# Performance work log

Hardware: AMD Instinct MI355X
Metric: run time of the kernel (lower is better)

Reference implementation:

```python
import jax, jax.numpy as jnp
import numpy as np

K = 8192
C = 512
BETA = 0.25
DECAY = 0.99
EPS = 1e-05


def setup_inputs() -> dict:
    key = jax.random.key(0)
    k1, k2, k3 = jax.random.split(key, 3)
    z_e = jax.random.normal(k1, (8, 1024, C), dtype=jnp.float32)
    codebook = jax.random.normal(k2, (K, C), dtype=jnp.float32) * 0.02
    cluster_size = jax.random.uniform(k3, (K,), dtype=jnp.float32)
    embed_avg = codebook  # buffer initialized as a copy of the codebook
    return {"z_e": z_e, "codebook": codebook, "cluster_size": cluster_size, "embed_avg": embed_avg}


def reference(z_e, codebook, cluster_size, embed_avg):
    B, N, Cc = z_e.shape
    z = z_e.reshape(-1, Cc)            # [T, C]
    z32 = z.astype(jnp.float32)
    cw = codebook.astype(jnp.float32)  # [K, C]

    # squared L2 distances: ||z||^2 - 2 z.e + ||e||^2  -> [T, K]
    dist = (jnp.sum(z32 * z32, axis=1, keepdims=True)
            - 2.0 * (z32 @ cw.T)
            + jnp.sum(cw * cw, axis=1)[None, :])
    idx = jnp.argmin(dist, axis=1)     # [T]
    z_q = cw[idx]                      # [T, C] gather

    vq_loss = BETA * jnp.mean((z32 - jax.lax.stop_gradient(z_q)) ** 2)

    # straight-through estimator
    z_st = z + jax.lax.stop_gradient(z_q.astype(z.dtype) - z)
    z_q_st = z_st.reshape(B, N, Cc)
    indices = idx.reshape(B, N)

    # EMA codebook update (training path; no_grad in original)
    counts = jax.ops.segment_sum(jnp.ones(idx.shape, jnp.float32), idx, num_segments=K)
    embed_sum = jax.ops.segment_sum(z32, idx, num_segments=K)  # [K, C] scatter-add
    new_cluster_size = cluster_size * DECAY + counts * (1.0 - DECAY)
    new_embed_avg = embed_avg * DECAY + embed_sum * (1.0 - DECAY)
    n = jnp.maximum(jnp.sum(new_cluster_size), 1.0)
    smoothed = (new_cluster_size + EPS) / (n + K * EPS) * n
    new_codebook = new_embed_avg / smoothed[:, None]

    return z_q_st, indices, vq_loss, new_codebook, new_cluster_size, new_embed_avg
```

## Files before the change

kernel.cpp:

```cpp
#include <hip/hip_runtime.h>
#include <cstdint>
#include <cstddef>

#define T_TOK 8192
#define K_CODE 8192
#define C_DIM 512
#define BETA 0.25f
#define DECAY 0.99f
#define ONE_MINUS_DECAY 0.01f
#define EPS_F 1e-5f
#define K_EPS 0.08192f
#define MARGIN 0.0625f

#define ZQ_OFF   ((size_t)0)
#define IDX_OFF  ((size_t)4194304)
#define LOSS_OFF ((size_t)4202496)
#define NCB_OFF  ((size_t)4202497)
#define NCS_OFF  ((size_t)8396801)
#define NEA_OFF  ((size_t)8404993)

#define CP_F_OFF    ((size_t)2097152)
#define SLAB1_F_OFF ((size_t)8404994)
#define SLAB2_F_OFF ((size_t)(8404994 + 524288))
#define LOSSP_F_OFF ((size_t)9453570)
#define LIST_I_OFF  ((size_t)10502146)
#define OFFSA_I_OFF ((size_t)10510338)
#define OFFSB_I_OFF ((size_t)10518530)

#define WS_ZNORM  0
#define WS_ENORM  8192
#define WS_ICOUNT 16384
#define WS_NSUM   24576

typedef _Float16 half8 __attribute__((ext_vector_type(8)));
typedef _Float16 half4v __attribute__((ext_vector_type(4)));
typedef float floatx4 __attribute__((ext_vector_type(4)));
typedef unsigned long long ull;

__device__ __forceinline__ void gload16(const void* g, void* l) {
    __builtin_amdgcn_global_load_lds(
        (const __attribute__((address_space(1))) void*)g,
        (__attribute__((address_space(3))) void*)l, 16, 0, 0);
}

__device__ __forceinline__ unsigned umin32(unsigned a, unsigned b) { return a < b ? a : b; }
__device__ __forceinline__ unsigned umax32(unsigned a, unsigned b) { return a > b ? a : b; }

__device__ __forceinline__ float dot8(float4 z0, float4 z1, float4 c0, float4 c1) {
    float p = 0.0f;
    p = fmaf(z0.x, c0.x, p); p = fmaf(z0.y, c0.y, p);
    p = fmaf(z0.z, c0.z, p); p = fmaf(z0.w, c0.w, p);
    p = fmaf(z1.x, c1.x, p); p = fmaf(z1.y, c1.y, p);
    p = fmaf(z1.z, c1.z, p); p = fmaf(z1.w, c1.w, p);
    return p;
}

__global__ __launch_bounds__(256) void prep_kernel(const float* __restrict__ z,
                                                   const float* __restrict__ cb,
                                                   _Float16* __restrict__ zp,
                                                   _Float16* __restrict__ cp,
                                                   float* __restrict__ ws) {
    int tid = threadIdx.x;
    int row = blockIdx.x * 2 + (tid >> 7);
    int l128 = tid & 127;
    const float* src;
    _Float16* dst;
    float* nrm;
    if (row < T_TOK) { src = z + (size_t)row * C_DIM; dst = zp + (size_t)row * C_DIM; nrm = ws + WS_ZNORM + row; }
    else { int r = row - T_TOK; src = cb + (size_t)r * C_DIM; dst = cp + (size_t)r * C_DIM; nrm = ws + WS_ENORM + r; }
    float4 v = *(const float4*)(src + l128 * 4);
    half4v h;
    h[0] = (_Float16)v.x; h[1] = (_Float16)v.y;
    h[2] = (_Float16)v.z; h[3] = (_Float16)v.w;
    *(half4v*)(dst + l128 * 4) = h;
    float s = v.x * v.x + v.y * v.y + v.z * v.z + v.w * v.w;
    #pragma unroll
    for (int m = 32; m; m >>= 1) s += __shfl_down(s, m, 64);
    __shared__ float red[4];
    if ((tid & 63) == 0) red[tid >> 6] = s;
    __syncthreads();
    if ((tid & 127) == 0) nrm[0] = red[tid >> 6] + red[(tid >> 6) + 1];
}

__global__ __launch_bounds__(256) void dist_mfma_kernel(
        const _Float16* __restrict__ zp, const _Float16* __restrict__ cp,
        const float* __restrict__ znorm, const float* __restrict__ enorm,
        unsigned* __restrict__ slab1, unsigned* __restrict__ slab2) {
    __shared__ __align__(16) _Float16 As[128 * 32];
    __shared__ __align__(16) _Float16 Bs[128 * 32];
    __shared__ unsigned red2[128][2][2];
    const int tid = threadIdx.x;
    const int w = tid >> 6, lane = tid & 63;
    const int quad = lane >> 4, lr = lane & 15;
    const int wm = w >> 1, wn = w & 1;

    const int GRID_N = 64, GROUP_M = 16;
    int pid = blockIdx.x;
    int per = GROUP_M * GRID_N;
    int g = pid / per;
    int local = pid % per;
    int bm = g * GROUP_M + (local & (GROUP_M - 1));
    int bn = local / GROUP_M;
    const int mBase = bm * 128, nBase = bn * 128;

    int r0 = (w * 2 + 0) * 16 + (lane >> 2);
    int r1 = (w * 2 + 1) * 16 + (lane >> 2);
    int cq = (((lane & 3) ^ ((lane >> 3) & 3))) * 8;
    const _Float16* ga0 = zp + (size_t)(mBase + r0) * C_DIM + cq;
    const _Float16* ga1 = zp + (size_t)(mBase + r1) * C_DIM + cq;
    const _Float16* gb0 = cp + (size_t)(nBase + r0) * C_DIM + cq;
    const _Float16* gb1 = cp + (size_t)(nBase + r1) * C_DIM + cq;
    _Float16* la0 = As + (w * 2 + 0) * 512;
    _Float16* la1 = As + (w * 2 + 1) * 512;
    _Float16* lb0 = Bs + (w * 2 + 0) * 512;
    _Float16* lb1 = Bs + (w * 2 + 1) * 512;

    const int slotA = (quad ^ ((lr >> 1) & 3)) * 8;
    const _Float16* aFrag = As + ((size_t)(wm * 64 + lr)) * 32 + slotA;
    const _Float16* bFrag = Bs + ((size_t)(wn * 64 + lr)) * 32 + slotA;

    floatx4 acc[4][4] = {};

    for (int it = 0; it < 16; ++it) {
        __syncthreads();
        gload16(ga0, la0);
        gload16(ga1, la1);
        gload16(gb0, lb0);
        gload16(gb1, lb1);
        ga0 += 32; ga1 += 32; gb0 += 32; gb1 += 32;
        __syncthreads();
        half8 af[4], bf[4];
        #pragma unroll
        for (int i = 0; i < 4; ++i) af[i] = *(const half8*)(aFrag + i * 16 * 32);
        #pragma unroll
        for (int j = 0; j < 4; ++j) bf[j] = *(const half8*)(bFrag + j * 16 * 32);
        #pragma unroll
        for (int i = 0; i < 4; ++i)
            #pragma unroll
            for (int j = 0; j < 4; ++j)
                acc[i][j] = __builtin_amdgcn_mfma_f32_16x16x32_f16(af[i], bf[j], acc[i][j], 0, 0, 0);
    }

    float en[4];
    #pragma unroll
    for (int j = 0; j < 4; ++j) en[j] = enorm[nBase + wn * 64 + j * 16 + lr];
    #pragma unroll
    for (int i = 0; i < 4; ++i) {
        #pragma unroll
        for (int r = 0; r < 4; ++r) {
            int lrow = wm * 64 + i * 16 + quad * 4 + r;
            float zn = znorm[mBase + lrow];
            unsigned t1 = 0xFFFFFFFFu, t2 = 0xFFFFFFFFu;
            #pragma unroll
            for (int j = 0; j < 4; ++j) {
                int nLoc = wn * 64 + j * 16 + lr;
                float s = (zn - 2.0f * acc[i][j][r]) + en[j];
                s = fmaxf(s, 0.0f);
                unsigned key = ((__float_as_uint(s) + 0x40u) & 0xFFFFFF80u) | (unsigned)nLoc;
                if (key < t1) { t2 = t1; t1 = key; } else if (key < t2) t2 = key;
            }
            #pragma unroll
            for (int msk = 1; msk < 16; msk <<= 1) {
                unsigned o1 = (unsigned)__shfl_xor((int)t1, msk, 64);
                unsigned o2 = (unsigned)__shfl_xor((int)t2, msk, 64);
                unsigned n1 = umin32(t1, o1);
                unsigned n2 = umin32(umax32(t1, o1), umin32(t2, o2));
                t1 = n1; t2 = n2;
            }
            if (lr == 0) { red2[lrow][wn][0] = t1; red2[lrow][wn][1] = t2; }
        }
    }
    __syncthreads();
    if (tid < 128) {
        unsigned a1 = red2[tid][0][0], a2 = red2[tid][0][1];
        unsigned b1 = red2[tid][1][0], b2 = red2[tid][1][1];
        unsigned m1 = umin32(a1, b1);
        unsigned m2 = umin32(umax32(a1, b1), umin32(a2, b2));
        slab1[(size_t)(mBase + tid) * 64 + bn] = m1;
        slab2[(size_t)(mBase + tid) * 64 + bn] = m2;
    }
}

__global__ __launch_bounds__(256) void refine_gather_kernel(
        const float* __restrict__ z, const float* __restrict__ cb,
        const float* __restrict__ znorm, const float* __restrict__ enorm,
        const unsigned* __restrict__ slab1, const unsigned* __restrict__ slab2,
        float* __restrict__ out, int* __restrict__ icount,
        float* __restrict__ lossP) {
    int tid = threadIdx.x;
    int wv = tid >> 6, lane = tid & 63;
    int t = blockIdx.x * 4 + wv;

    unsigned s1 = slab1[(size_t)t * 64 + lane];
    unsigned s2 = slab2[(size_t)t * 64 + lane];
    const float* zr = z + (size_t)t * C_DIM + lane * 8;
    float4 z0 = *(const float4*)zr;
    float4 z1 = *(const float4*)(zr + 4);

    unsigned v = s1;
    #pragma unroll
    for (int m = 32; m; m >>= 1) v = umin32(v, (unsigned)__shfl_xor((int)v, m, 64));
    float thr = __uint_as_float(v & 0xFFFFFF80u) + MARGIN;
    float d1 = __uint_as_float(s1 & 0xFFFFFF80u);
    float d2 = __uint_as_float(s2 & 0xFFFFFF80u);
    bool full = d2 < thr;
    ull fullMask = __ballot(full);
    ull singleMask = __ballot(!full && d1 < thr);

    float zn = znorm[t];
    ull lbest = ~0ull;

    while (fullMask) {
        int bn = __builtin_ctzll(fullMask);
        fullMask &= fullMask - 1;
        int nb = bn * 128;
        for (int rep = 0; rep < 32; ++rep) {
            int n0 = nb + rep * 4;
            const float* cr0 = cb + (size_t)(n0    ) * C_DIM + lane * 8;
            const float* cr1 = cb + (size_t)(n0 + 1) * C_DIM + lane * 8;
            const float* cr2 = cb + (size_t)(n0 + 2) * C_DIM + lane * 8;
            const float* cr3 = cb + (size_t)(n0 + 3) * C_DIM + lane * 8;
            float4 c00 = *(const float4*)cr0, c01 = *(const float4*)(cr0 + 4);
            float4 c10 = *(const float4*)cr1, c11 = *(const float4*)(cr1 + 4);
            float4 c20 = *(const float4*)cr2, c21 = *(const float4*)(cr2 + 4);
            float4 c30 = *(const float4*)cr3, c31 = *(const float4*)(cr3 + 4);
            float p0 = dot8(z0, z1, c00, c01);
            float p1 = dot8(z0, z1, c10, c11);
            float p2 = dot8(z0, z1, c20, c21);
            float p3 = dot8(z0, z1, c30, c31);
            #pragma unroll
            for (int m = 32; m; m >>= 1) {
                p0 += __shfl_xor(p0, m, 64);
                p1 += __shfl_xor(p1, m, 64);
                p2 += __shfl_xor(p2, m, 64);
                p3 += __shfl_xor(p3, m, 64);
            }
            float s0 = (zn - 2.0f * p0) + enorm[n0];
            float s1f = (zn - 2.0f * p1) + enorm[n0 + 1];
            float s2f = (zn - 2.0f * p2) + enorm[n0 + 2];
            float s3f = (zn - 2.0f * p3) + enorm[n0 + 3];
            ull k0 = ((ull)__float_as_uint(s0) << 32) | (unsigned)(n0);
            ull k1 = ((ull)__float_as_uint(s1f) << 32) | (unsigned)(n0 + 1);
            ull k2 = ((ull)__float_as_uint(s2f) << 32) | (unsigned)(n0 + 2);
            ull k3 = ((ull)__float_as_uint(s3f) << 32) | (unsigned)(n0 + 3);
            ull kk = k0 < k1 ? k0 : k1;
            ull kl = k2 < k3 ? k2 : k3;
            kk = kk < kl ? kk : kl;
            lbest = lbest < kk ? lbest : kk;
        }
    }
    while (singleMask) {
        int bn = __builtin_ctzll(singleMask);
        singleMask &= singleMask - 1;
        int n = bn * 128 + (__shfl((int)s1, bn, 64) & 0x7F);
        const float* cr = cb + (size_t)n * C_DIM + lane * 8;
        float4 c0 = *(const float4*)cr;
        float4 c1 = *(const float4*)(cr + 4);
        float p = dot8(z0, z1, c0, c1);
        #pragma unroll
        for (int m = 32; m; m >>= 1) p += __shfl_xor(p, m, 64);
        float s = (zn - 2.0f * p) + enorm[n];
        ull pk = ((ull)__float_as_uint(s) << 32) | (unsigned)n;
        lbest = lbest < pk ? lbest : pk;
    }
    int idx = (int)(unsigned)(lbest & 0xFFFFFFFFull);

    const float* qr = cb + (size_t)idx * C_DIM + lane * 8;
    float4 q0 = *(const float4*)qr;
    float4 q1 = *(const float4*)(qr + 4);
    float4 o0, o1;
    o0.x = z0.x + (q0.x - z0.x); o0.y = z0.y + (q0.y - z0.y);
    o0.z = z0.z + (q0.z - z0.z); o0.w = z0.w + (q0.w - z0.w);
    o1.x = z1.x + (q1.x - z1.x); o1.y = z1.y + (q1.y - z1.y);
    o1.z = z1.z + (q1.z - z1.z); o1.w = z1.w + (q1.w - z1.w);
    float* zq = out + ZQ_OFF + (size_t)t * C_DIM + lane * 8;
    *(float4*)zq = o0;
    *(float4*)(zq + 4) = o1;
    float d, l = 0.0f;
    d = z0.x - q0.x; l = fmaf(d, d, l);
    d = z0.y - q0.y; l = fmaf(d, d, l);
    d = z0.z - q0.z; l = fmaf(d, d, l);
    d = z0.w - q0.w; l = fmaf(d, d, l);
    d = z1.x - q1.x; l = fmaf(d, d, l);
    d = z1.y - q1.y; l = fmaf(d, d, l);
    d = z1.z - q1.z; l = fmaf(d, d, l);
    d = z1.w - q1.w; l = fmaf(d, d, l);
    #pragma unroll
    for (int m = 32; m; m >>= 1) l += __shfl_down(l, m, 64);
    if (lane == 0) {
        lossP[t] = l * (BETA / ((float)T_TOK * (float)C_DIM));
        out[IDX_OFF + t] = (float)idx;
        atomicAdd(&icount[idx], 1);
    }
}

__global__ __launch_bounds__(256) void scan_ncs_kernel(
        const int* __restrict__ icount, const float* __restrict__ cs,
        const float* __restrict__ lossP,
        int* __restrict__ offsA, int* __restrict__ offsB,
        float* __restrict__ out, float* __restrict__ nsum) {
    __shared__ int tot[256];
    int tid = threadIdx.x;
    int v[32];
    int s = 0;
    float ncsSum = 0.0f, lsum = 0.0f;
    #pragma unroll
    for (int j = 0; j < 32; ++j) {
        int k = tid * 32 + j;
        int x = icount[k];
        v[j] = s;
        s += x;
        float ncs = cs[k] * DECAY + (float)x * ONE_MINUS_DECAY;
        out[NCS_OFF + k] = ncs;
        ncsSum += ncs;
        lsum += lossP[k];
    }
    tot[tid] = s;
    __syncthreads();
    for (int d = 1; d < 256; d <<= 1) {
        int x = (tid >= d) ? tot[tid - d] : 0;
        __syncthreads();
        tot[tid] += x;
        __syncthreads();
    }
    int excl = tid ? tot[tid - 1] : 0;
    #pragma unroll
    for (int j = 0; j < 32; ++j) {
        int o = excl + v[j];
        offsA[tid * 32 + j] = o;
        offsB[tid * 32 + j] = o;
    }
    float a = ncsSum, l = lsum;
    #pragma unroll
    for (int m = 32; m; m >>= 1) { a += __shfl_down(a, m, 64); l += __shfl_down(l, m, 64); }
    __shared__ float redA[4], redL[4];
    if ((tid & 63) == 0) { redA[tid >> 6] = a; redL[tid >> 6] = l; }
    __syncthreads();
    if (tid == 0) {
        nsum[0] = (redA[0] + redA[1]) + (redA[2] + redA[3]);
        out[LOSS_OFF] = (redL[0] + redL[1]) + (redL[2] + redL[3]);
    }
}

__global__ __launch_bounds__(256) void scatter_kernel(const float* __restrict__ out,
                                                      int* __restrict__ offsA,
                                                      int* __restrict__ list) {
    int t = blockIdx.x * 256 + threadIdx.x;
    int idx = (int)out[IDX_OFF + t];
    int slot = atomicAdd(&offsA[idx], 1);
    list[slot] = t;
}

__global__ __launch_bounds__(256) void percode_sum_kernel(
        const float* __restrict__ z, const int* __restrict__ list,
        const int* __restrict__ offsB, const int* __restrict__ icount,
        float* __restrict__ out) {
    int k = blockIdx.x;
    int tid = threadIdx.x;
    int off = offsB[k], cnt = icount[k];
    float a0 = 0.0f, a1 = 0.0f;
    for (int i = 0; i < cnt; ++i) {
        int t = list[off + i];
        const float* zrow = z + (size_t)t * C_DIM;
        a0 += zrow[tid];
        a1 += zrow[tid + 256];
    }
    out[NCB_OFF + (size_t)k * C_DIM + tid] = a0;
    out[NCB_OFF + (size_t)k * C_DIM + tid + 256] = a1;
}

__global__ __launch_bounds__(256) void finalize_kernel(const float* __restrict__ ea,
                                                       float* __restrict__ out,
                                                       const float* __restrict__ nsumP) {
    int k = blockIdx.x;
    int tid = threadIdx.x;
    float n = fmaxf(*nsumP, 1.0f);
    float ncs = out[NCS_OFF + k];
    float smoothed = ((ncs + EPS_F) / (n + K_EPS)) * n;
    #pragma unroll
    for (int s = 0; s < 2; ++s) {
        int c = tid + s * 256;
        size_t o = (size_t)k * C_DIM + c;
        float es = out[NCB_OFF + o];
        float nea = ea[o] * DECAY + es * ONE_MINUS_DECAY;
        out[NEA_OFF + o] = nea;
        out[NCB_OFF + o] = nea / smoothed;
    }
}

extern "C" void kernel_launch(void* const* d_in, const int* in_sizes, int n_in,
                              void* d_out, int out_size, void* d_ws, size_t ws_size,
                              hipStream_t stream) {
    const float* z  = (const float*)d_in[0];
    const float* cb = (const float*)d_in[1];
    const float* cs = (const float*)d_in[2];
    const float* ea = (const float*)d_in[3];
    float* out = (float*)d_out;
    float* ws  = (float*)d_ws;
    _Float16* zp = (_Float16*)out;
    _Float16* cp = (_Float16*)(out + CP_F_OFF);
    float* lossP = out + LOSSP_F_OFF;
    unsigned* slab1 = (unsigned*)(out + SLAB1_F_OFF);
    unsigned* slab2 = (unsigned*)(out + SLAB2_F_OFF);
    int* list  = (int*)(out + LIST_I_OFF);
    int* offsA = (int*)(out + OFFSA_I_OFF);
    int* offsB = (int*)(out + OFFSB_I_OFF);
    int* icount = (int*)(ws + WS_ICOUNT);
    float* nsum = ws + WS_NSUM;

    hipMemsetAsync(ws + WS_ICOUNT, 0, (size_t)8192 * 4, stream);

    prep_kernel<<<8192, 256, 0, stream>>>(z, cb, zp, cp, ws);
    dist_mfma_kernel<<<4096, 256, 0, stream>>>(zp, cp, ws + WS_ZNORM, ws + WS_ENORM, slab1, slab2);
    refine_gather_kernel<<<2048, 256, 0, stream>>>(z, cb, ws + WS_ZNORM, ws + WS_ENORM,
                                                   slab1, slab2, out, icount, lossP);
    scan_ncs_kernel<<<1, 256, 0, stream>>>(icount, cs, lossP, offsA, offsB, out, nsum);
    scatter_kernel<<<32, 256, 0, stream>>>(out, offsA, list);
    percode_sum_kernel<<<8192, 256, 0, stream>>>(z, list, offsB, icount, out);
    finalize_kernel<<<8192, 256, 0, stream>>>(ea, out, nsum);
}
```

Measured before the change: 273.0 us.

## Fuse scatter into scan kernel with LDS atomics and remap dist block order for XCDs

Merges the separate scatter kernel into the single-block scan kernel, keeping per-code write offsets in shared memory and using LDS atomics instead of global atomics. This removes one kernel launch and a global offsets buffer. It also remaps the distance kernel's block index so consecutive hardware block IDs (round-robined across the 8 XCDs) map to contiguous grouped tiles per XCD, aiming to improve L2 reuse. The scatter now runs on one block, serializing 8192 tokens through 256 threads.

```diff
diff --git a/kernel.cpp b/kernel.cpp
--- a/kernel.cpp
+++ b/kernel.cpp
@@ -24,7 +24,6 @@
 #define SLAB2_F_OFF ((size_t)(8404994 + 524288))
 #define LOSSP_F_OFF ((size_t)9453570)
 #define LIST_I_OFF  ((size_t)10502146)
-#define OFFSA_I_OFF ((size_t)10510338)
 #define OFFSB_I_OFF ((size_t)10518530)
 
 #define WS_ZNORM  0
@@ -95,7 +94,8 @@
     const int wm = w >> 1, wn = w & 1;
 
     const int GRID_N = 64, GROUP_M = 16;
-    int pid = blockIdx.x;
+    int pid0 = blockIdx.x;
+    int pid = (pid0 & 7) * 512 + (pid0 >> 3);
     int per = GROUP_M * GRID_N;
     int g = pid / per;
     int local = pid % per;
@@ -294,12 +294,13 @@
     }
 }
 
-__global__ __launch_bounds__(256) void scan_ncs_kernel(
+__global__ __launch_bounds__(256) void scan_ncs_scatter_kernel(
         const int* __restrict__ icount, const float* __restrict__ cs,
-        const float* __restrict__ lossP,
-        int* __restrict__ offsA, int* __restrict__ offsB,
+        const float* __restrict__ lossP, const float* __restrict__ outIdx,
+        int* __restrict__ offsB, int* __restrict__ list,
         float* __restrict__ out, float* __restrict__ nsum) {
     __shared__ int tot[256];
+    __shared__ int ofs[8192];
     int tid = threadIdx.x;
     int v[32];
     int s = 0;
@@ -326,9 +327,17 @@
     int excl = tid ? tot[tid - 1] : 0;
     #pragma unroll
     for (int j = 0; j < 32; ++j) {
+        int k = tid * 32 + j;
         int o = excl + v[j];
-        offsA[tid * 32 + j] = o;
-        offsB[tid * 32 + j] = o;
+        ofs[k] = o;
+        offsB[k] = o;
+    }
+    __syncthreads();
+    for (int base = 0; base < T_TOK; base += 256) {
+        int t = base + tid;
+        int idx = (int)outIdx[t];
+        int slot = atomicAdd(&ofs[idx], 1);
+        list[slot] = t;
     }
     float a = ncsSum, l = lsum;
     #pragma unroll
@@ -340,15 +349,6 @@
         nsum[0] = (redA[0] + redA[1]) + (redA[2] + redA[3]);
         out[LOSS_OFF] = (redL[0] + redL[1]) + (redL[2] + redL[3]);
     }
-}
-
-__global__ __launch_bounds__(256) void scatter_kernel(const float* __restrict__ out,
-                                                      int* __restrict__ offsA,
-                                                      int* __restrict__ list) {
-    int t = blockIdx.x * 256 + threadIdx.x;
-    int idx = (int)out[IDX_OFF + t];
-    int slot = atomicAdd(&offsA[idx], 1);
-    list[slot] = t;
 }
 
 __global__ __launch_bounds__(256) void percode_sum_kernel(
@@ -403,7 +403,6 @@
     unsigned* slab1 = (unsigned*)(out + SLAB1_F_OFF);
     unsigned* slab2 = (unsigned*)(out + SLAB2_F_OFF);
     int* list  = (int*)(out + LIST_I_OFF);
-    int* offsA = (int*)(out + OFFSA_I_OFF);
     int* offsB = (int*)(out + OFFSB_I_OFF);
     int* icount = (int*)(ws + WS_ICOUNT);
     float* nsum = ws + WS_NSUM;
@@ -414,8 +413,8 @@
     dist_mfma_kernel<<<4096, 256, 0, stream>>>(zp, cp, ws + WS_ZNORM, ws + WS_ENORM, slab1, slab2);
     refine_gather_kernel<<<2048, 256, 0, stream>>>(z, cb, ws + WS_ZNORM, ws + WS_ENORM,
                                                    slab1, slab2, out, icount, lossP);
-    scan_ncs_kernel<<<1, 256, 0, stream>>>(icount, cs, lossP, offsA, offsB, out, nsum);
-    scatter_kernel<<<32, 256, 0, stream>>>(out, offsA, list);
+    scan_ncs_scatter_kernel<<<1, 256, 0, stream>>>(icount, cs, lossP, out + IDX_OFF,
+                                                   offsB, list, out, nsum);
     percode_sum_kernel<<<8192, 256, 0, stream>>>(z, list, offsB, icount, out);
     finalize_kernel<<<8192, 256, 0, stream>>>(ea, out, nsum);
 }
```

Result: no change. 275.2 us (+0.8%).
